# Optimization experiments

Hardware: AMD Instinct MI355X
Metric: run time of the kernel (lower is better)

Reference implementation:

```python
import jax, jax.numpy as jnp
import numpy as np

ALPHA = 1.0          # gating temperature (train_alpha=False)
DEPTH = 4            # floor(log2(leaves=16))
LEAF_NUM = 16        # 2**DEPTH
N_INTERNAL = LEAF_NUM - 2  # nodes 1..14 (root handled separately)
B, D, OUT = 8192, 512, 64


def _prob(x, pw, aW, ab):
    # vectorized Node.prob with set_comps=True (comparators recomputed from batch mean)
    comp = -jnp.mean(x * pw, axis=0)                      # [in]
    dist = jax.nn.sigmoid(ALPHA * (pw * x + comp))        # [B, in]
    attn = jax.nn.softmax(x @ aW.T + ab, axis=-1)         # [B, in]
    return jnp.sum(dist * attn, axis=1, keepdims=True)    # [B, 1]


def setup_inputs() -> dict:
    key = jax.random.key(0)
    ks = jax.random.split(key, 12)
    s = 0.02
    return {
        "x": jax.random.normal(ks[0], (B, D), jnp.float32),
        # root node (input_size=D, output_size=D)
        "calc_W0": jax.random.normal(ks[1], (D, D), jnp.float32) * s,
        "calc_b0": jnp.zeros((D,), jnp.float32),
        "prob_w0": jax.random.uniform(ks[2], (D,), jnp.float32),
        "attn_W0": jax.random.normal(ks[3], (D, D), jnp.float32) * s,
        "attn_b0": jnp.zeros((D,), jnp.float32),
        # internal nodes 1..14 (input_size=2D, output_size=D), stacked
        "calc_W": jax.random.normal(ks[4], (N_INTERNAL, D, 2 * D), jnp.float32) * s,
        "calc_b": jnp.zeros((N_INTERNAL, D), jnp.float32),
        "prob_w": jax.random.uniform(ks[5], (N_INTERNAL, 2 * D), jnp.float32),
        "attn_W": jax.random.normal(ks[6], (N_INTERNAL, 2 * D, 2 * D), jnp.float32) * s,
        "attn_b": jnp.zeros((N_INTERNAL, 2 * D), jnp.float32),
        # leaf nodes: learned output vectors (torch.rand init)
        "leaf_out": jax.random.uniform(ks[7], (LEAF_NUM, OUT), jnp.float32),
    }


def reference(x, calc_W0, calc_b0, prob_w0, attn_W0, attn_b0,
              calc_W, calc_b, prob_w, attn_W, attn_b, leaf_out):
    outs, probab = {}, {}
    # root
    outs[0] = jax.nn.relu(x @ calc_W0.T + calc_b0)            # [B, D]
    p = _prob(x, prob_w0, attn_W0, attn_b0)                   # [B, 1]
    probab[1] = 1.0 - p
    probab[2] = p
    # internal nodes 1..leaf_num-2 (binary-tree routing)
    for n in range(1, LEAF_NUM - 1):
        parent = (n - 1) // 2
        inp = jnp.concatenate([outs[parent], x], axis=1)      # [B, 2D]
        outs[n] = jax.nn.relu(inp @ calc_W[n - 1].T + calc_b[n - 1])
        p = _prob(inp, prob_w[n - 1], attn_W[n - 1], attn_b[n - 1])
        probab[2 * n + 1] = probab[n] * (1.0 - p)
        probab[2 * n + 2] = probab[n] * p
    # leaves: indices LEAF_NUM-1 .. 2*LEAF_NUM-2
    leaf_p = jnp.concatenate([probab[i + LEAF_NUM - 1] for i in range(LEAF_NUM)], axis=1)  # [B, 16]
    # sum over leaves of probab * leaf_out == leaf_p @ leaf_out
    actions = leaf_p @ leaf_out                                # [B, OUT]
    return jax.nn.softmax(actions, axis=-1)
```

## Files before the change

kernel.cpp:

```cpp
#include <hip/hip_runtime.h>
#include <hip/hip_bf16.h>
#include <cstdint>


#define NROWS 8192
#define HALFD 512

typedef __bf16 bf16x8 __attribute__((ext_vector_type(8)));
typedef short  short8 __attribute__((ext_vector_type(8)));
typedef float  f32x4  __attribute__((ext_vector_type(4)));

union FragU { short8 s; bf16x8 b; };

struct GArgs {
  const __hip_bfloat16* A0[4];
  const __hip_bfloat16* Bw[4];
  const float* bias[4];
  const float* pw[4];
  const float* cm0[4];
  __hip_bfloat16* outB[4];
  float* csOut[4];
  float* S1[4];
  float* S2[4];
  int mode[4];
  int gx[4];
  int K[4];
};

__device__ __forceinline__ void gl2lds16(const void* g, void* l) {
  __builtin_amdgcn_global_load_lds((__attribute__((address_space(1))) void*)g,
                                   (__attribute__((address_space(3))) void*)l,
                                   16, 0, 0);
}

struct CvtArgs { const float* src[5]; __hip_bfloat16* dst[5]; int nblk[5]; };
__global__ void k_cvt(CvtArgs a) {
  int b = blockIdx.x, r = 0;
  while (b >= a.nblk[r]) { b -= a.nblk[r]; ++r; }
  const int i = (b * 256 + threadIdx.x) * 4;
  float4 v = *(const float4*)(a.src[r] + i);
  union { short4 s4; __hip_bfloat16 h[4]; } u;
  u.h[0] = __float2bfloat16(v.x);
  u.h[1] = __float2bfloat16(v.y);
  u.h[2] = __float2bfloat16(v.z);
  u.h[3] = __float2bfloat16(v.w);
  *(short4*)(a.dst[r] + i) = u.s4;
}

__global__ void k_colsum_f32(const float* __restrict__ src, float* __restrict__ dst) {
  int c  = blockIdx.x * 256 + threadIdx.x;
  int r0 = blockIdx.y * 256;
  float s = 0.f;
  for (int r = 0; r < 256; ++r) s += src[(size_t)(r0 + r) * HALFD + c];
  atomicAdd(&dst[c], s);
}

__global__ __launch_bounds__(256, 2)
void k_gemm(GArgs ga, const __hip_bfloat16* __restrict__ A1,
            const float* __restrict__ cm1) {
  __shared__ alignas(16) short As[128 * 64];
  __shared__ alignas(16) short Bs[128 * 64];

  const int z = blockIdx.z;
  const int id  = blockIdx.x + gridDim.x * blockIdx.y;
  const int xcd = id & 7;
  const int q   = id >> 3;
  const int bx  = q >> 3;
  const int by  = xcd * 8 + (q & 7);
  if (bx >= ga.gx[z]) return;

  const __hip_bfloat16* __restrict__ Ah0 = ga.A0[z];
  const __hip_bfloat16* __restrict__ Bw  = ga.Bw[z];
  const float* __restrict__ bias = ga.bias[z];
  const int K = ga.K[z];

  const int tid  = threadIdx.x;
  const int lane = tid & 63;
  const int wv   = tid >> 6;
  const int wm   = wv >> 1, wn = wv & 1;
  const int lr   = lane & 15, lg = lane >> 4;
  const int row0 = by * 128;
  const int col0 = bx * 128;

  f32x4 acc[4][4];
#pragma unroll
  for (int i = 0; i < 4; ++i)
#pragma unroll
    for (int j = 0; j < 4; ++j)
#pragma unroll
      for (int e = 0; e < 4; ++e) acc[i][j][e] = 0.f;

  const int sr = tid >> 3;
  const int sc = (((tid & 7) ^ (sr & 7)) << 3);
  const int sw = lr & 7;

  for (int kt = 0; kt < K; kt += 64) {
    const __hip_bfloat16* Asrc = (kt < HALFD) ? Ah0 : A1;
    const int kl = kt & (HALFD - 1);
    __syncthreads();
#pragma unroll
    for (int rnd = 0; rnd < 4; ++rnd) {
      const int r = rnd * 32 + sr;
      gl2lds16(Asrc + (size_t)(row0 + r) * HALFD + kl + sc,
               (char*)As + rnd * 4096 + wv * 1024);
      gl2lds16(Bw + (size_t)(col0 + r) * K + kt + sc,
               (char*)Bs + rnd * 4096 + wv * 1024);
    }
    __syncthreads();
#pragma unroll
    for (int kk = 0; kk < 64; kk += 32) {
      FragU a[4], b[4];
#pragma unroll
      for (int mi = 0; mi < 4; ++mi)
        a[mi].s = *(const short8*)(As + (wm * 64 + mi * 16 + lr) * 64 +
                                   ((((kk >> 3) + lg) ^ sw) << 3));
#pragma unroll
      for (int ni = 0; ni < 4; ++ni)
        b[ni].s = *(const short8*)(Bs + (wn * 64 + ni * 16 + lr) * 64 +
                                   ((((kk >> 3) + lg) ^ sw) << 3));
#pragma unroll
      for (int mi = 0; mi < 4; ++mi)
#pragma unroll
        for (int ni = 0; ni < 4; ++ni)
          acc[mi][ni] = __builtin_amdgcn_mfma_f32_16x16x32_bf16(a[mi].b, b[ni].b,
                                                               acc[mi][ni], 0, 0, 0);
    }
  }

  if (ga.mode[z] == 0) {
    __hip_bfloat16* outB = ga.outB[z];
    float* csOut = ga.csOut[z];
#pragma unroll
    for (int ni = 0; ni < 4; ++ni) {
      const int col  = col0 + wn * 64 + ni * 16 + lr;
      const float bv = bias[col];
      __hip_bfloat16* op = outB + (size_t)(col >> 9) * ((size_t)NROWS * HALFD) + (col & 511);
      float csum = 0.f;
#pragma unroll
      for (int mi = 0; mi < 4; ++mi) {
#pragma unroll
        for (int rg = 0; rg < 4; ++rg) {
          const int row = row0 + wm * 64 + mi * 16 + lg * 4 + rg;
          float v = acc[mi][ni][rg] + bv;
          v = v > 0.f ? v : 0.f;
          csum += v;
          op[(size_t)row * HALFD] = __float2bfloat16(v);
        }
      }
      csum += __shfl_xor(csum, 16);
      csum += __shfl_xor(csum, 32);
      if (lg == 0) atomicAdd(&csOut[col], csum);
    }
  } else {
    const float* __restrict__ pw  = ga.pw[z];
    const float* __restrict__ cm0 = ga.cm0[z];
    const int node = col0 >> 10;
    float* s1p = ga.S1[z] + (size_t)node * NROWS;
    float* s2p = ga.S2[z] + (size_t)node * NROWS;
    float bv[4], pwv[4], cmv[4];
    const __hip_bfloat16* Ain[4];
#pragma unroll
    for (int ni = 0; ni < 4; ++ni) {
      const int col = col0 + wn * 64 + ni * 16 + lr;
      bv[ni]  = bias[col];
      pwv[ni] = pw[col];
      const int ii   = col & 1023;
      const int half = ii >> 9;
      const int cc   = ii & 511;
      cmv[ni] = (half ? cm1[cc] : cm0[cc]) * (1.f / 8192.f);
      Ain[ni] = (half ? A1 : Ah0) + cc;
    }
#pragma unroll
    for (int mi = 0; mi < 4; ++mi) {
#pragma unroll
      for (int rg = 0; rg < 4; ++rg) {
        const int row = row0 + wm * 64 + mi * 16 + lg * 4 + rg;
        float s1 = 0.f, s2 = 0.f;
#pragma unroll
        for (int ni = 0; ni < 4; ++ni) {
          const float l = acc[mi][ni][rg] + bv[ni];
          const float e = __expf(l);
          const float inpv = __bfloat162float(Ain[ni][(size_t)row * HALFD]);
          const float zz = pwv[ni] * (inpv - cmv[ni]);
          const float dist = 1.f / (1.f + __expf(-zz));
          s1 += e;
          s2 += dist * e;
        }
#pragma unroll
        for (int off = 1; off < 16; off <<= 1) {
          s1 += __shfl_xor(s1, off);
          s2 += __shfl_xor(s2, off);
        }
        if (lr == 0) {
          atomicAdd(&s1p[row], s1);
          atomicAdd(&s2p[row], s2);
        }
      }
    }
  }
}

__global__ void k_finalize(const float* __restrict__ S1, const float* __restrict__ S2,
                           const float* __restrict__ leaf_out, float* __restrict__ out) {
  const int r    = (blockIdx.x * 256 + threadIdx.x) >> 6;
  const int lane = threadIdx.x & 63;
  float pb[31];
  pb[0] = 1.f;
#pragma unroll
  for (int n = 0; n < 15; ++n) {
    const float p = S2[(size_t)n * NROWS + r] / S1[(size_t)n * NROWS + r];
    pb[2 * n + 1] = pb[n] * (1.f - p);
    pb[2 * n + 2] = pb[n] * p;
  }
  float a = 0.f;
#pragma unroll
  for (int i = 0; i < 16; ++i) a += pb[15 + i] * leaf_out[i * 64 + lane];
  float m = a;
#pragma unroll
  for (int off = 1; off < 64; off <<= 1) m = fmaxf(m, __shfl_xor(m, off));
  const float e = __expf(a - m);
  float s = e;
#pragma unroll
  for (int off = 1; off < 64; off <<= 1) s += __shfl_xor(s, off);
  out[(size_t)r * 64 + lane] = e / s;
}

static constexpr size_t O_S1   = 0;
static constexpr size_t O_S2   = O_S1 + (size_t)15 * NROWS * 4;
static constexpr size_t O_XSUM = O_S2 + (size_t)15 * NROWS * 4;
static constexpr size_t O_CS   = O_XSUM + 512 * 4;
static constexpr size_t O_ZEND = O_CS + 7 * 512 * 4;
static constexpr size_t O_XB   = O_ZEND;
static constexpr size_t O_OUTS = O_XB + (size_t)NROWS * HALFD * 2;
static constexpr size_t O_CW0  = O_OUTS + 7 * (size_t)NROWS * HALFD * 2;
static constexpr size_t O_AW0  = O_CW0 + (size_t)512 * 512 * 2;
static constexpr size_t O_CW   = O_AW0 + (size_t)512 * 512 * 2;
static constexpr size_t O_AW   = O_CW + (size_t)14 * 512 * 1024 * 2;

extern "C" void kernel_launch(void* const* d_in, const int* in_sizes, int n_in,
                              void* d_out, int out_size, void* d_ws, size_t ws_size,
                              hipStream_t stream) {
  const float* x        = (const float*)d_in[0];
  const float* calc_b0  = (const float*)d_in[2];
  const float* prob_w0  = (const float*)d_in[3];
  const float* attn_b0  = (const float*)d_in[5];
  const float* calc_b   = (const float*)d_in[7];
  const float* prob_w   = (const float*)d_in[8];
  const float* attn_b   = (const float*)d_in[10];
  const float* leaf_out = (const float*)d_in[11];
  float* out = (float*)d_out;
  char* ws = (char*)d_ws;

  float* S1   = (float*)(ws + O_S1);
  float* S2   = (float*)(ws + O_S2);
  float* xsum = (float*)(ws + O_XSUM);
  float* cs   = (float*)(ws + O_CS);
  __hip_bfloat16* xb   = (__hip_bfloat16*)(ws + O_XB);
  __hip_bfloat16* outs = (__hip_bfloat16*)(ws + O_OUTS);
  __hip_bfloat16* cW0b = (__hip_bfloat16*)(ws + O_CW0);
  __hip_bfloat16* aW0b = (__hip_bfloat16*)(ws + O_AW0);
  __hip_bfloat16* cWb  = (__hip_bfloat16*)(ws + O_CW);
  __hip_bfloat16* aWb  = (__hip_bfloat16*)(ws + O_AW);
  const size_t OSZ = (size_t)NROWS * HALFD;

  hipMemsetAsync(d_ws, 0, O_ZEND, stream);

  {
    CvtArgs ca{};
    ca.src[0] = x;                     ca.dst[0] = xb;   ca.nblk[0] = NROWS * HALFD / 1024;
    ca.src[1] = (const float*)d_in[1]; ca.dst[1] = cW0b; ca.nblk[1] = 512 * 512 / 1024;
    ca.src[2] = (const float*)d_in[4]; ca.dst[2] = aW0b; ca.nblk[2] = 512 * 512 / 1024;
    ca.src[3] = (const float*)d_in[6]; ca.dst[3] = cWb;  ca.nblk[3] = 14 * 512 * 1024 / 1024;
    ca.src[4] = (const float*)d_in[9]; ca.dst[4] = aWb;  ca.nblk[4] = 14 * 1024 * 1024 / 1024;
    int tot = ca.nblk[0] + ca.nblk[1] + ca.nblk[2] + ca.nblk[3] + ca.nblk[4];
    k_cvt<<<tot, 256, 0, stream>>>(ca);
  }
  k_colsum_f32<<<dim3(2, 32), 256, 0, stream>>>(x, xsum);

  {
    GArgs ga{};
    ga.mode[0] = 0; ga.gx[0] = 4; ga.K[0] = 512;
    ga.A0[0] = xb; ga.Bw[0] = cW0b; ga.bias[0] = calc_b0;
    ga.outB[0] = outs; ga.csOut[0] = cs;
    ga.mode[1] = 1; ga.gx[1] = 4; ga.K[1] = 512;
    ga.A0[1] = xb; ga.Bw[1] = aW0b; ga.bias[1] = attn_b0;
    ga.pw[1] = prob_w0; ga.cm0[1] = xsum;
    ga.S1[1] = S1; ga.S2[1] = S2;
    k_gemm<<<dim3(4, 64, 2), 256, 0, stream>>>(ga, xb, xsum);
  }
  {
    GArgs ga{};
    ga.mode[0] = 0; ga.gx[0] = 8; ga.K[0] = 1024;
    ga.A0[0] = outs; ga.Bw[0] = cWb; ga.bias[0] = calc_b;
    ga.outB[0] = outs + OSZ; ga.csOut[0] = cs + 512;
    ga.mode[1] = 1; ga.gx[1] = 16; ga.K[1] = 1024;
    ga.A0[1] = outs; ga.Bw[1] = aWb; ga.bias[1] = attn_b;
    ga.pw[1] = prob_w; ga.cm0[1] = cs;
    ga.S1[1] = S1 + (size_t)1 * NROWS; ga.S2[1] = S2 + (size_t)1 * NROWS;
    k_gemm<<<dim3(16, 64, 2), 256, 0, stream>>>(ga, xb, xsum);
  }
  {
    GArgs ga{};
    for (int i = 0; i < 2; ++i) {
      ga.mode[i] = 0; ga.gx[i] = 8; ga.K[i] = 1024;
      ga.A0[i] = outs + (size_t)(1 + i) * OSZ;
      ga.Bw[i] = cWb + (size_t)(2 + 2 * i) * 512 * 1024;
      ga.bias[i] = calc_b + (2 + 2 * i) * 512;
      ga.outB[i] = outs + (size_t)(3 + 2 * i) * OSZ;
      ga.csOut[i] = cs + (size_t)(3 + 2 * i) * 512;
    }
    for (int i = 0; i < 2; ++i) {
      const int zi = 2 + i;
      ga.mode[zi] = 1; ga.gx[zi] = 16; ga.K[zi] = 1024;
      ga.A0[zi] = outs + (size_t)(1 + i) * OSZ;
      ga.Bw[zi] = aWb + (size_t)(2 + 2 * i) * 1024 * 1024;
      ga.bias[zi] = attn_b + (2 + 2 * i) * 1024;
      ga.pw[zi] = prob_w + (2 + 2 * i) * 1024;
      ga.cm0[zi] = cs + (size_t)(1 + i) * 512;
      ga.S1[zi] = S1 + (size_t)(3 + 2 * i) * NROWS;
      ga.S2[zi] = S2 + (size_t)(3 + 2 * i) * NROWS;
    }
    k_gemm<<<dim3(16, 64, 4), 256, 0, stream>>>(ga, xb, xsum);
  }
  {
    GArgs ga{};
    for (int i = 0; i < 4; ++i) {
      ga.mode[i] = 1; ga.gx[i] = 16; ga.K[i] = 1024;
      ga.A0[i] = outs + (size_t)(3 + i) * OSZ;
      ga.Bw[i] = aWb + (size_t)(6 + 2 * i) * 1024 * 1024;
      ga.bias[i] = attn_b + (6 + 2 * i) * 1024;
      ga.pw[i] = prob_w + (6 + 2 * i) * 1024;
      ga.cm0[i] = cs + (size_t)(3 + i) * 512;
      ga.S1[i] = S1 + (size_t)(7 + 2 * i) * NROWS;
      ga.S2[i] = S2 + (size_t)(7 + 2 * i) * NROWS;
    }
    k_gemm<<<dim3(16, 64, 4), 256, 0, stream>>>(ga, xb, xsum);
  }

  k_finalize<<<NROWS * 64 / 256, 256, 0, stream>>>(S1, S2, leaf_out, out);
}
```

Measured before the change: 579.5 us.

## Use 256x256 tiles with double-buffered LDS and interleaved MFMA/load schedule

```diff
diff --git a/kernel.cpp b/kernel.cpp
--- a/kernel.cpp
+++ b/kernel.cpp
@@ -55,75 +55,138 @@
   atomicAdd(&dst[c], s);
 }
 
-__global__ __launch_bounds__(256, 2)
+
+#define DS_A(BUF, MQ) do { \
+  _Pragma("unroll") for (int i_ = 0; i_ < 4; ++i_) \
+  _Pragma("unroll") for (int k_ = 0; k_ < 2; ++k_) \
+    a[i_][k_].s = *(const short8*)(&As[BUF][wm][((MQ)*64 + i_*16 + lr)*64 + \
+                                   (((k_*4 + lg) ^ sw) << 3)]); \
+} while (0)
+
+#define DS_B(BUF, NQ) do { \
+  _Pragma("unroll") for (int j_ = 0; j_ < 2; ++j_) \
+  _Pragma("unroll") for (int k_ = 0; k_ < 2; ++k_) \
+    b[(NQ)*2 + j_][k_].s = *(const short8*)(&Bs[BUF][nh][(bro + ((NQ)*2 + j_)*16 + lr)*64 + \
+                                             (((k_*4 + lg) ^ sw) << 3)]); \
+} while (0)
+
+#define MFMA_Q(MQ, NQ) do { \
+  _Pragma("unroll") for (int i_ = 0; i_ < 4; ++i_) \
+  _Pragma("unroll") for (int j_ = 0; j_ < 2; ++j_) \
+  _Pragma("unroll") for (int k_ = 0; k_ < 2; ++k_) \
+    acc[(MQ)*4 + i_][(NQ)*2 + j_] = __builtin_amdgcn_mfma_f32_16x16x32_bf16( \
+        a[i_][k_].b, b[(NQ)*2 + j_][k_].b, acc[(MQ)*4 + i_][(NQ)*2 + j_], 0, 0, 0); \
+} while (0)
+
+#define STG_A(DB, H, L) gl2lds16(aS + (size_t)(((H)*128 + (L)*64) * HALFD), \
+                                 (char*)(&As[DB][H][0]) + (L)*8192 + wvB)
+#define STG_B(DB, H, L) gl2lds16(bS + (size_t)((H)*128 + (L)*64) * (size_t)K, \
+                                 (char*)(&Bs[DB][H][0]) + (L)*8192 + wvB)
+
+#define TILE_BODY(BUF, DB, STG) do { \
+   \
+  DS_A(BUF, 0); DS_B(BUF, 0); \
+  if (STG) { STG_A(DB, 0, 0); STG_A(DB, 1, 0); } \
+  __builtin_amdgcn_s_barrier(); \
+  asm volatile("s_waitcnt lgkmcnt(0)"); \
+  __builtin_amdgcn_s_setprio(1); MFMA_Q(0, 0); __builtin_amdgcn_s_setprio(0); \
+  __builtin_amdgcn_s_barrier(); \
+   \
+  DS_B(BUF, 1); \
+  if (STG) { STG_B(DB, 0, 0); STG_B(DB, 0, 1); \
+             asm volatile("s_waitcnt vmcnt(4)" ::: "memory"); } \
+  else     { asm volatile("s_waitcnt vmcnt(0)" ::: "memory"); } \
+  __builtin_amdgcn_s_barrier(); \
+  asm volatile("s_waitcnt lgkmcnt(0)"); \
+  __builtin_amdgcn_s_setprio(1); MFMA_Q(0, 1); __builtin_amdgcn_s_setprio(0); \
+  __builtin_amdgcn_s_barrier(); \
+   \
+  DS_A(BUF, 1); \
+  if (STG) { STG_B(DB, 1, 0); STG_B(DB, 1, 1); } \
+  __builtin_amdgcn_s_barrier(); \
+  asm volatile("s_waitcnt lgkmcnt(0)"); \
+  __builtin_amdgcn_s_setprio(1); MFMA_Q(1, 0); __builtin_amdgcn_s_setprio(0); \
+  __builtin_amdgcn_s_barrier(); \
+   \
+  if (STG) { STG_A(DB, 0, 1); STG_A(DB, 1, 1); \
+             asm volatile("s_waitcnt vmcnt(2)" ::: "memory"); } \
+  __builtin_amdgcn_s_barrier(); \
+  __builtin_amdgcn_s_setprio(1); MFMA_Q(1, 1); __builtin_amdgcn_s_setprio(0); \
+  __builtin_amdgcn_s_barrier(); \
+} while (0)
+
+__global__ __launch_bounds__(512, 2)
 void k_gemm(GArgs ga, const __hip_bfloat16* __restrict__ A1,
             const float* __restrict__ cm1) {
-  __shared__ alignas(16) short As[128 * 64];
-  __shared__ alignas(16) short Bs[128 * 64];
+  __shared__ alignas(16) short As[2][2][128 * 64];
+  __shared__ alignas(16) short Bs[2][2][128 * 64];
 
   const int z = blockIdx.z;
   const int id  = blockIdx.x + gridDim.x * blockIdx.y;
   const int xcd = id & 7;
   const int q   = id >> 3;
-  const int bx  = q >> 3;
-  const int by  = xcd * 8 + (q & 7);
+  const int bx  = q >> 2;
+  const int by  = xcd * 4 + (q & 3);
   if (bx >= ga.gx[z]) return;
 
   const __hip_bfloat16* __restrict__ Ah0 = ga.A0[z];
   const __hip_bfloat16* __restrict__ Bw  = ga.Bw[z];
   const float* __restrict__ bias = ga.bias[z];
-  const int K = ga.K[z];
+  const int K  = ga.K[z];
+  const int NT = K >> 6;
 
   const int tid  = threadIdx.x;
   const int lane = tid & 63;
   const int wv   = tid >> 6;
-  const int wm   = wv >> 1, wn = wv & 1;
+  const int wm   = wv >> 2, wn = wv & 3;
   const int lr   = lane & 15, lg = lane >> 4;
-  const int row0 = by * 128;
-  const int col0 = bx * 128;
-
-  f32x4 acc[4][4];
-#pragma unroll
-  for (int i = 0; i < 4; ++i)
+  const int sw   = lr & 7;
+  const int nh   = wn >> 1;
+  const int bro  = (wn & 1) * 64;
+  const int wvB  = wv * 1024;
+  const int row0 = by * 256;
+  const int col0 = bx * 256;
+
+  const int sr = tid >> 3;
+  const int gc = (tid & 7) ^ (sr & 7);
+  const size_t aoff = (size_t)(row0 + sr) * HALFD + gc * 8;
+  const size_t boff = (size_t)(col0 + sr) * (size_t)K + gc * 8;
+
+  f32x4 acc[8][4];
+#pragma unroll
+  for (int i = 0; i < 8; ++i)
 #pragma unroll
     for (int j = 0; j < 4; ++j)
 #pragma unroll
       for (int e = 0; e < 4; ++e) acc[i][j][e] = 0.f;
 
-  const int sr = tid >> 3;
-  const int sc = (((tid & 7) ^ (sr & 7)) << 3);
-  const int sw = lr & 7;
-
-  for (int kt = 0; kt < K; kt += 64) {
-    const __hip_bfloat16* Asrc = (kt < HALFD) ? Ah0 : A1;
-    const int kl = kt & (HALFD - 1);
-    __syncthreads();
-#pragma unroll
-    for (int rnd = 0; rnd < 4; ++rnd) {
-      const int r = rnd * 32 + sr;
-      gl2lds16(Asrc + (size_t)(row0 + r) * HALFD + kl + sc,
-               (char*)As + rnd * 4096 + wv * 1024);
-      gl2lds16(Bw + (size_t)(col0 + r) * K + kt + sc,
-               (char*)Bs + rnd * 4096 + wv * 1024);
-    }
-    __syncthreads();
-#pragma unroll
-    for (int kk = 0; kk < 64; kk += 32) {
-      FragU a[4], b[4];
-#pragma unroll
-      for (int mi = 0; mi < 4; ++mi)
-        a[mi].s = *(const short8*)(As + (wm * 64 + mi * 16 + lr) * 64 +
-                                   ((((kk >> 3) + lg) ^ sw) << 3));
-#pragma unroll
-      for (int ni = 0; ni < 4; ++ni)
-        b[ni].s = *(const short8*)(Bs + (wn * 64 + ni * 16 + lr) * 64 +
-                                   ((((kk >> 3) + lg) ^ sw) << 3));
-#pragma unroll
-      for (int mi = 0; mi < 4; ++mi)
-#pragma unroll
-        for (int ni = 0; ni < 4; ++ni)
-          acc[mi][ni] = __builtin_amdgcn_mfma_f32_16x16x32_bf16(a[mi].b, b[ni].b,
-                                                               acc[mi][ni], 0, 0, 0);
+  FragU a[4][2], b[4][2];
+
+  const __hip_bfloat16* aS = Ah0 + aoff;
+  const __hip_bfloat16* bS = Bw + boff;
+
+  STG_A(0, 0, 0); STG_A(0, 1, 0);
+  STG_B(0, 0, 0); STG_B(0, 0, 1);
+  STG_B(0, 1, 0); STG_B(0, 1, 1);
+  STG_A(0, 0, 1); STG_A(0, 1, 1);
+  asm volatile("s_waitcnt vmcnt(2)" ::: "memory");
+  __builtin_amdgcn_s_barrier();
+
+  for (int tt = 0; tt < NT; tt += 2) {
+    {
+      const int sn = tt + 1;
+      aS = ((sn < 8) ? Ah0 : A1) + ((sn & 7) << 6) + aoff;
+      bS = Bw + sn * 64 + boff;
+      TILE_BODY(0, 1, 1);
+    }
+    {
+      const int sn = tt + 2;
+      const int stg = (sn < NT);
+      if (stg) {
+        aS = ((sn < 8) ? Ah0 : A1) + ((sn & 7) << 6) + aoff;
+        bS = Bw + sn * 64 + boff;
+      }
+      TILE_BODY(1, 0, stg);
     }
   }
 
@@ -137,10 +200,10 @@
       __hip_bfloat16* op = outB + (size_t)(col >> 9) * ((size_t)NROWS * HALFD) + (col & 511);
       float csum = 0.f;
 #pragma unroll
-      for (int mi = 0; mi < 4; ++mi) {
+      for (int mi = 0; mi < 8; ++mi) {
 #pragma unroll
         for (int rg = 0; rg < 4; ++rg) {
-          const int row = row0 + wm * 64 + mi * 16 + lg * 4 + rg;
+          const int row = row0 + wm * 128 + mi * 16 + lg * 4 + rg;
           float v = acc[mi][ni][rg] + bv;
           v = v > 0.f ? v : 0.f;
           csum += v;
@@ -171,10 +234,10 @@
       Ain[ni] = (half ? A1 : Ah0) + cc;
     }
 #pragma unroll
-    for (int mi = 0; mi < 4; ++mi) {
+    for (int mi = 0; mi < 8; ++mi) {
 #pragma unroll
       for (int rg = 0; rg < 4; ++rg) {
-        const int row = row0 + wm * 64 + mi * 16 + lg * 4 + rg;
+        const int row = row0 + wm * 128 + mi * 16 + lg * 4 + rg;
         float s1 = 0.f, s2 = 0.f;
 #pragma unroll
         for (int ni = 0; ni < 4; ++ni) {
@@ -279,30 +342,30 @@
 
   {
     GArgs ga{};
-    ga.mode[0] = 0; ga.gx[0] = 4; ga.K[0] = 512;
+    ga.mode[0] = 0; ga.gx[0] = 2; ga.K[0] = 512;
     ga.A0[0] = xb; ga.Bw[0] = cW0b; ga.bias[0] = calc_b0;
     ga.outB[0] = outs; ga.csOut[0] = cs;
-    ga.mode[1] = 1; ga.gx[1] = 4; ga.K[1] = 512;
+    ga.mode[1] = 1; ga.gx[1] = 2; ga.K[1] = 512;
     ga.A0[1] = xb; ga.Bw[1] = aW0b; ga.bias[1] = attn_b0;
     ga.pw[1] = prob_w0; ga.cm0[1] = xsum;
     ga.S1[1] = S1; ga.S2[1] = S2;
-    k_gemm<<<dim3(4, 64, 2), 256, 0, stream>>>(ga, xb, xsum);
+    k_gemm<<<dim3(2, 32, 2), 512, 0, stream>>>(ga, xb, xsum);
   }
   {
     GArgs ga{};
-    ga.mode[0] = 0; ga.gx[0] = 8; ga.K[0] = 1024;
+    ga.mode[0] = 0; ga.gx[0] = 4; ga.K[0] = 1024;
     ga.A0[0] = outs; ga.Bw[0] = cWb; ga.bias[0] = calc_b;
     ga.outB[0] = outs + OSZ; ga.csOut[0] = cs + 512;
-    ga.mode[1] = 1; ga.gx[1] = 16; ga.K[1] = 1024;
+    ga.mode[1] = 1; ga.gx[1] = 8; ga.K[1] = 1024;
     ga.A0[1] = outs; ga.Bw[1] = aWb; ga.bias[1] = attn_b;
     ga.pw[1] = prob_w; ga.cm0[1] = cs;
     ga.S1[1] = S1 + (size_t)1 * NROWS; ga.S2[1] = S2 + (size_t)1 * NROWS;
-    k_gemm<<<dim3(16, 64, 2), 256, 0, stream>>>(ga, xb, xsum);
+    k_gemm<<<dim3(8, 32, 2), 512, 0, stream>>>(ga, xb, xsum);
   }
   {
     GArgs ga{};
     for (int i = 0; i < 2; ++i) {
-      ga.mode[i] = 0; ga.gx[i] = 8; ga.K[i] = 1024;
+      ga.mode[i] = 0; ga.gx[i] = 4; ga.K[i] = 1024;
       ga.A0[i] = outs + (size_t)(1 + i) * OSZ;
       ga.Bw[i] = cWb + (size_t)(2 + 2 * i) * 512 * 1024;
       ga.bias[i] = calc_b + (2 + 2 * i) * 512;
@@ -311,7 +374,7 @@
     }
     for (int i = 0; i < 2; ++i) {
       const int zi = 2 + i;
-      ga.mode[zi] = 1; ga.gx[zi] = 16; ga.K[zi] = 1024;
+      ga.mode[zi] = 1; ga.gx[zi] = 8; ga.K[zi] = 1024;
       ga.A0[zi] = outs + (size_t)(1 + i) * OSZ;
       ga.Bw[zi] = aWb + (size_t)(2 + 2 * i) * 1024 * 1024;
       ga.bias[zi] = attn_b + (2 + 2 * i) * 1024;
@@ -320,12 +383,12 @@
       ga.S1[zi] = S1 + (size_t)(3 + 2 * i) * NROWS;
       ga.S2[zi] = S2 + (size_t)(3 + 2 * i) * NROWS;
     }
-    k_gemm<<<dim3(16, 64, 4), 256, 0, stream>>>(ga, xb, xsum);
+    k_gemm<<<dim3(8, 32, 4), 512, 0, stream>>>(ga, xb, xsum);
   }
   {
     GArgs ga{};
     for (int i = 0; i < 4; ++i) {
-      ga.mode[i] = 1; ga.gx[i] = 16; ga.K[i] = 1024;
+      ga.mode[i] = 1; ga.gx[i] = 8; ga.K[i] = 1024;
       ga.A0[i] = outs + (size_t)(3 + i) * OSZ;
       ga.Bw[i] = aWb + (size_t)(6 + 2 * i) * 1024 * 1024;
       ga.bias[i] = attn_b + (6 + 2 * i) * 1024;
@@ -334,7 +397,7 @@
       ga.S1[i] = S1 + (size_t)(7 + 2 * i) * NROWS;
       ga.S2[i] = S2 + (size_t)(7 + 2 * i) * NROWS;
     }
-    k_gemm<<<dim3(16, 64, 4), 256, 0, stream>>>(ga, xb, xsum);
+    k_gemm<<<dim3(8, 32, 4), 512, 0, stream>>>(ga, xb, xsum);
   }
 
   k_finalize<<<NROWS * 64 / 256, 256, 0, stream>>>(S1, S2, leaf_out, out);
```

Measured after the change: 641.7 us. 10.7% more time.
